# Optimization experiments

Measured on AMD Instinct MI355X. Metric: run time of the kernel, lower is better.

## Reference

```python
import jax, jax.numpy as jnp
import numpy as np


def _conv1x1(x, W, b):
    # 1x1 conv == per-pixel linear: x [B,H,W,Cin] @ W [Cin,Cout] + b
    return jnp.einsum('bhwc,cd->bhwd', x, W) + b


def setup_inputs() -> dict:
    key = jax.random.key(0)
    ks = jax.random.split(key, 5)
    B, H, W, C = 4, 64, 64, 256
    Ck = C // 8
    x = jax.random.normal(ks[0], (B, H, W, C), dtype=jnp.float32)
    Wf = jax.random.normal(ks[1], (C, Ck), dtype=jnp.float32) * 0.05
    Wg = jax.random.normal(ks[2], (C, Ck), dtype=jnp.float32) * 0.05
    Wh = jax.random.normal(ks[3], (C, C), dtype=jnp.float32) * 0.05
    Wv = jax.random.normal(ks[4], (C, C), dtype=jnp.float32) * 0.05
    return {
        'x': x,
        'Wf': Wf, 'bf': jnp.zeros((Ck,), jnp.float32),
        'Wg': Wg, 'bg': jnp.zeros((Ck,), jnp.float32),
        'Wh': Wh, 'bh': jnp.zeros((C,), jnp.float32),
        'Wv': Wv, 'bv': jnp.zeros((C,), jnp.float32),
    }


def reference(x, Wf, bf, Wg, bg, Wh, bh, Wv, bv):
    B, H, W, C = x.shape
    f = _conv1x1(x, Wf, bf).reshape(B, H * W, -1)   # [B,N,C/8]
    g = _conv1x1(x, Wg, bg).reshape(B, H * W, -1)   # [B,N,C/8]
    hm = _conv1x1(x, Wh, bh).reshape(B, H * W, C)   # [B,N,C]
    # unscaled attention: s = g @ f^T, softmax over last axis
    s = jnp.einsum('bnk,bmk->bnm', g, f)            # [B,N,N]
    beta = jax.nn.softmax(s, axis=-1)
    o = jnp.einsum('bnm,bmc->bnc', beta, hm)        # [B,N,C]
    o = o.reshape(B, H, W, C)
    o = _conv1x1(o, Wv, bv)
    return x + o
```

## Files before the change

### kernel.cpp

```cpp
#include <hip/hip_runtime.h>
#include <math.h>


typedef unsigned short u16;
typedef __attribute__((ext_vector_type(8))) short  bf16x8;
typedef __attribute__((ext_vector_type(4))) float  f32x4;

__device__ inline u16 f2bf(float x) {
    unsigned u = __float_as_uint(x);
    unsigned r = (u + 0x7fffu + ((u >> 16) & 1u)) >> 16;
    return (u16)r;
}

__device__ inline float bf2f(short s) {
    return __uint_as_float(((unsigned)(u16)s) << 16);
}

__device__ inline bf16x8 cvt8(float4 a, float4 b) {
    bf16x8 r;
    r[0] = (short)f2bf(a.x); r[1] = (short)f2bf(a.y);
    r[2] = (short)f2bf(a.z); r[3] = (short)f2bf(a.w);
    r[4] = (short)f2bf(b.x); r[5] = (short)f2bf(b.y);
    r[6] = (short)f2bf(b.z); r[7] = (short)f2bf(b.w);
    return r;
}

#define ASYNC_CP16(gp, lp)                                                     \
    __builtin_amdgcn_global_load_lds(                                          \
        (const __attribute__((address_space(1))) void*)(gp),                   \
        (__attribute__((address_space(3))) void*)(lp), 16, 0, 0)

#define LOG2E 1.4426950408889634f

__device__ inline size_t vfrag_off(int b, int cg, int kc, int quad, int l16) {
    return ((((size_t)b * 16 + cg) * 128 + kc) << 9) + (quad << 7) + (l16 << 3);
}

__global__ __launch_bounds__(256) void prep_w2(
    const float* __restrict__ Wf, const float* __restrict__ Wg,
    const float* __restrict__ Wh, const float* __restrict__ Wv,
    u16* __restrict__ wT)
{
    __shared__ float ldsw[256 * 33];

    const int bid = blockIdx.x;
    const int t   = threadIdx.x;

    const float* src;
    int cs, c0, nbase;
    float scale = 1.f;
    if (bid == 0)       { src = Wf; cs = 32;  c0 = 0;               nbase = 0; }
    else if (bid == 1)  { src = Wg; cs = 32;  c0 = 0;               nbase = 32;  scale = LOG2E; }
    else if (bid < 10)  { src = Wh; cs = 256; c0 = (bid - 2) * 32;  nbase = 64  + (bid - 2) * 32; }
    else                { src = Wv; cs = 256; c0 = (bid - 10) * 32; nbase = 320 + (bid - 10) * 32; }

#pragma unroll
    for (int i = 0; i < 32; ++i) {
        int idx = i * 256 + t;
        int k = idx >> 5;
        int n = idx & 31;
        ldsw[k * 33 + n] = src[(size_t)k * cs + c0 + n];
    }
    __syncthreads();

#pragma unroll
    for (int i = 0; i < 32; ++i) {
        int idx = i * 256 + t;
        int n = idx >> 8;
        int k = idx & 255;
        wT[(size_t)(nbase + n) * 256 + k] = f2bf(ldsw[k * 33 + n] * scale);
    }
}

__global__ __launch_bounds__(256) void proj_mfma2(
    const float* __restrict__ x, const u16* __restrict__ wT,
    const float* __restrict__ bfv, const float* __restrict__ bgv,
    const float* __restrict__ bhv,
    u16* __restrict__ fg, u16* __restrict__ hmt)
{
    __shared__ float xl[16 * 268];

    const int t    = threadIdx.x;
    const int w    = t >> 6;
    const int lane = t & 63;
    const int quad = lane >> 4;
    const int l16  = lane & 15;
    const int m0   = blockIdx.x * 16;
    const int wb   = w * 80;

#pragma unroll
    for (int i = 0; i < 4; ++i) {
        int idx = i * 256 + t;
        int row = idx >> 6;
        int c4  = (idx & 63) << 2;
        float4 v = *reinterpret_cast<const float4*>(
            x + (size_t)(m0 + row) * 256 + c4);
        *reinterpret_cast<float4*>(&xl[row * 268 + c4]) = v;
    }
    __syncthreads();

    f32x4 acc[5];
#pragma unroll
    for (int nt = 0; nt < 5; ++nt)
#pragma unroll
        for (int r = 0; r < 4; ++r) acc[nt][r] = 0.f;

#pragma unroll 2
    for (int ks = 0; ks < 8; ++ks) {
        const float* xp = &xl[l16 * 268 + ks * 32 + quad * 8];
        float4 a0 = *reinterpret_cast<const float4*>(xp);
        float4 a1 = *reinterpret_cast<const float4*>(xp + 4);
        bf16x8 afrag = cvt8(a0, a1);
#pragma unroll
        for (int nt = 0; nt < 5; ++nt) {
            bf16x8 bfrag = *reinterpret_cast<const bf16x8*>(
                wT + (size_t)(wb + nt * 16 + l16) * 256 + ks * 32 + quad * 8);
            acc[nt] = __builtin_amdgcn_mfma_f32_16x16x32_bf16(
                afrag, bfrag, acc[nt], 0, 0, 0);
        }
    }

    const int bb   = m0 >> 12;
    const int npix = m0 & 4095;
#pragma unroll
    for (int nt = 0; nt < 5; ++nt) {
        int col = wb + nt * 16 + l16;
        if (col < 64) {
            float bias = (col < 32) ? bfv[col] : bgv[col - 32] * LOG2E;
            int row = m0 + quad * 4;
#pragma unroll
            for (int r = 0; r < 4; ++r)
                fg[(size_t)(row + r) * 64 + col] = f2bf(acc[nt][r] + bias);
        } else {
            int c = col - 64;
            float bias = bhv[c];
            int n0 = npix + quad * 4;
            ushort4 hv;
            hv.x = f2bf(acc[nt][0] + bias);
            hv.y = f2bf(acc[nt][1] + bias);
            hv.z = f2bf(acc[nt][2] + bias);
            hv.w = f2bf(acc[nt][3] + bias);
            size_t off = ((((size_t)bb * 16 + (c >> 4)) * 128 + (n0 >> 5))
                          << 9) + (((n0 >> 3) & 3) << 7) + ((c & 15) << 3) +
                         (n0 & 7);
            *reinterpret_cast<ushort4*>(hmt + off) = hv;
        }
    }
}

__global__ __launch_bounds__(256) void attn5(
    const u16* __restrict__ fg, const u16* __restrict__ hmt,
    u16* __restrict__ obf, float* __restrict__ lpart, int ksl)
{
    __shared__ u16 fl[2][4096];
    __shared__ u16 pl[8192];

    const int t    = threadIdx.x;
    const int w    = t >> 6;
    const int lane = t & 63;
    const int quad = lane >> 4;
    const int l16  = lane & 15;

    int b, qt, ks;
    if (ksl == 1) {
        const int u   = blockIdx.x;
        const int xcd = u & 7;
        b = xcd >> 1;
        const int v = ((u >> 3) << 1) | (xcd & 1);
        qt = v >> 1;
        ks = v & 1;
    } else {
        ks = 0;
        qt = blockIdx.x & 63;
        b  = blockIdx.x >> 6;
    }
    const int nkt = 32 >> ksl;
    const int kt0 = ks * nkt;

    const size_t fg_base = (size_t)b * 4096 * 64;

    const bf16x8 gfrag = *reinterpret_cast<const bf16x8*>(
        fg + fg_base + (size_t)(qt * 64 + w * 16 + l16) * 64 + 32 + quad * 8);

    f32x4 oacc[4][4];
#pragma unroll
    for (int mt = 0; mt < 4; ++mt)
#pragma unroll
        for (int nt = 0; nt < 4; ++nt)
#pragma unroll
            for (int r = 0; r < 4; ++r) oacc[mt][nt][r] = 0.f;

    float lsum[4] = {0.f, 0.f, 0.f, 0.f};
    const f32x4 zero4 = {0.f, 0.f, 0.f, 0.f};

    {
        const u16* gp = fg + fg_base +
            (size_t)(kt0 * 128 + (2 * w) * 16 + l16) * 64 + quad * 8;
        ASYNC_CP16(gp, &fl[0][(2 * w) * 512]);
        ASYNC_CP16(gp + 16 * 64, &fl[0][(2 * w + 1) * 512]);
    }

    for (int it = 0; it < nkt; ++it) {
        const int kt  = kt0 + it;
        const int buf = it & 1;
        __syncthreads();

        bf16x8 vbr[4][4];
#pragma unroll
        for (int nt = 0; nt < 4; ++nt)
#pragma unroll
            for (int kh = 0; kh < 4; ++kh)
                vbr[nt][kh] = *reinterpret_cast<const bf16x8*>(
                    hmt + vfrag_off(b, w * 4 + nt, kt * 4 + kh, quad, l16));

        if (it + 1 < nkt) {
            const u16* gp = fg + fg_base +
                (size_t)((kt + 1) * 128 + (2 * w) * 16 + l16) * 64 + quad * 8;
            ASYNC_CP16(gp, &fl[buf ^ 1][(2 * w) * 512]);
            ASYNC_CP16(gp + 16 * 64, &fl[buf ^ 1][(2 * w + 1) * 512]);
        }

        f32x4 sacc[8];
#pragma unroll
        for (int ct = 0; ct < 8; ++ct) {
            bf16x8 fb = *reinterpret_cast<const bf16x8*>(
                &fl[buf][ct * 512 + quad * 128 + l16 * 8]);
            sacc[ct] = __builtin_amdgcn_mfma_f32_16x16x32_bf16(
                gfrag, fb, zero4, 0, 0, 0);
        }

#pragma unroll
        for (int ct = 0; ct < 8; ++ct) {
#pragma unroll
            for (int r = 0; r < 4; ++r) {
                float p = __builtin_amdgcn_exp2f(sacc[ct][r]);
                lsum[r] += p;
                int row = w * 16 + quad * 4 + r;
                int key = ct * 16 + l16;
                pl[(key >> 3) * 512 + row * 8 + (key & 7)] = f2bf(p);
            }
        }
        __syncthreads();

#pragma unroll
        for (int kh = 0; kh < 4; ++kh) {
            bf16x8 pa[4];
#pragma unroll
            for (int mt = 0; mt < 4; ++mt)
                pa[mt] = *reinterpret_cast<const bf16x8*>(
                    &pl[(kh * 4 + quad) * 512 + (mt * 16 + l16) * 8]);
#pragma unroll
            for (int nt = 0; nt < 4; ++nt)
#pragma unroll
                for (int mt = 0; mt < 4; ++mt)
                    oacc[mt][nt] = __builtin_amdgcn_mfma_f32_16x16x32_bf16(
                        pa[mt], vbr[nt][kh], oacc[mt][nt], 0, 0, 0);
        }
    }

#pragma unroll
    for (int r = 0; r < 4; ++r) {
        float s = lsum[r];
        s += __shfl_xor(s, 1);
        s += __shfl_xor(s, 2);
        s += __shfl_xor(s, 4);
        s += __shfl_xor(s, 8);
        lsum[r] = s;
    }
    if (l16 == 0) {
#pragma unroll
        for (int r = 0; r < 4; ++r)
            lpart[((size_t)ks << 14) + b * 4096 + qt * 64 + w * 16 +
                  quad * 4 + r] = lsum[r];
    }

#pragma unroll
    for (int mt = 0; mt < 4; ++mt) {
        const int row16 = b * 256 + qt * 4 + mt;
#pragma unroll
        for (int nt = 0; nt < 4; ++nt) {
            int ksc = w * 2 + (nt >> 1);
            int qc  = (nt & 1) * 2 + (l16 >> 3);
            u16* op = obf + ((size_t)ks << 22) +
                (((size_t)row16 * 8 + ksc) << 9) + (qc << 7) + (l16 & 7);
#pragma unroll
            for (int r = 0; r < 4; ++r)
                op[(quad * 4 + r) * 8] = f2bf(oacc[mt][nt][r]);
        }
    }
}

__global__ __launch_bounds__(256, 2) void attn8(
    const u16* __restrict__ fg, const u16* __restrict__ hmt,
    u16* __restrict__ obf, float* __restrict__ lpart, int ksl)
{
    __shared__ u16 fl[2][4096];
    __shared__ u16 pl[16 * 1024];

    const int t    = threadIdx.x;
    const int w    = t >> 6;
    const int lane = t & 63;
    const int quad = lane >> 4;
    const int l16  = lane & 15;

    const int u   = blockIdx.x;
    const int xcd = u & 7;
    const int b   = xcd >> 1;
    const int v   = ((u >> 3) << 1) | (xcd & 1);
    const int qt  = v >> ksl;
    const int ks  = v & ((1 << ksl) - 1);

    const int nkt = 32 >> ksl;
    const int kt0 = ks * nkt;

    const size_t fg_base = (size_t)b * 4096 * 64;

    bf16x8 gfrag[2];
#pragma unroll
    for (int h2 = 0; h2 < 2; ++h2)
        gfrag[h2] = *reinterpret_cast<const bf16x8*>(
            fg + fg_base +
            (size_t)(qt * 128 + w * 32 + h2 * 16 + l16) * 64 + 32 + quad * 8);

    f32x4 oacc[8][4];
#pragma unroll
    for (int mt = 0; mt < 8; ++mt)
#pragma unroll
        for (int nt = 0; nt < 4; ++nt)
#pragma unroll
            for (int r = 0; r < 4; ++r) oacc[mt][nt][r] = 0.f;

    float lsum[2][4] = {{0.f, 0.f, 0.f, 0.f}, {0.f, 0.f, 0.f, 0.f}};
    const f32x4 zero4 = {0.f, 0.f, 0.f, 0.f};

    {
        const u16* gp = fg + fg_base +
            (size_t)(kt0 * 128 + (2 * w) * 16 + l16) * 64 + quad * 8;
        ASYNC_CP16(gp, &fl[0][(2 * w) * 512]);
        ASYNC_CP16(gp + 16 * 64, &fl[0][(2 * w + 1) * 512]);
    }

    for (int it = 0; it < nkt; ++it) {
        const int kt  = kt0 + it;
        const int buf = it & 1;
        __syncthreads();

        if (it + 1 < nkt) {
            const u16* gp = fg + fg_base +
                (size_t)((kt + 1) * 128 + (2 * w) * 16 + l16) * 64 + quad * 8;
            ASYNC_CP16(gp, &fl[buf ^ 1][(2 * w) * 512]);
            ASYNC_CP16(gp + 16 * 64, &fl[buf ^ 1][(2 * w + 1) * 512]);
        }

        {
            f32x4 sacc[8];
#pragma unroll
            for (int ct = 0; ct < 8; ++ct) {
                bf16x8 fb = *reinterpret_cast<const bf16x8*>(
                    &fl[buf][ct * 512 + quad * 128 + l16 * 8]);
                sacc[ct] = __builtin_amdgcn_mfma_f32_16x16x32_bf16(
                    gfrag[0], fb, zero4, 0, 0, 0);
            }
#pragma unroll
            for (int ct = 0; ct < 8; ++ct) {
#pragma unroll
                for (int r = 0; r < 4; ++r) {
                    float p = __builtin_amdgcn_exp2f(sacc[ct][r]);
                    lsum[0][r] += p;
                    int row = w * 32 + quad * 4 + r;
                    int key = ct * 16 + l16;
                    pl[(key >> 3) * 1024 + row * 8 + (key & 7)] = f2bf(p);
                }
            }
        }

        bf16x8 va[4][2];
#pragma unroll
        for (int nt = 0; nt < 4; ++nt)
#pragma unroll
            for (int j = 0; j < 2; ++j)
                va[nt][j] = *reinterpret_cast<const bf16x8*>(
                    hmt + vfrag_off(b, w * 4 + nt, kt * 4 + j, quad, l16));

        {
            f32x4 sacc[8];
#pragma unroll
            for (int ct = 0; ct < 8; ++ct) {
                bf16x8 fb = *reinterpret_cast<const bf16x8*>(
                    &fl[buf][ct * 512 + quad * 128 + l16 * 8]);
                sacc[ct] = __builtin_amdgcn_mfma_f32_16x16x32_bf16(
                    gfrag[1], fb, zero4, 0, 0, 0);
            }
#pragma unroll
            for (int ct = 0; ct < 8; ++ct) {
#pragma unroll
                for (int r = 0; r < 4; ++r) {
                    float p = __builtin_amdgcn_exp2f(sacc[ct][r]);
                    lsum[1][r] += p;
                    int row = w * 32 + 16 + quad * 4 + r;
                    int key = ct * 16 + l16;
                    pl[(key >> 3) * 1024 + row * 8 + (key & 7)] = f2bf(p);
                }
            }
        }
        __syncthreads();

#pragma unroll
        for (int kh = 0; kh < 2; ++kh) {
#pragma unroll
            for (int mh = 0; mh < 2; ++mh) {
                bf16x8 pa[4];
#pragma unroll
                for (int m = 0; m < 4; ++m)
                    pa[m] = *reinterpret_cast<const bf16x8*>(
                        &pl[(kh * 4 + quad) * 1024 +
                            ((mh * 4 + m) * 16 + l16) * 8]);
#pragma unroll
                for (int nt = 0; nt < 4; ++nt)
#pragma unroll
                    for (int m = 0; m < 4; ++m)
                        oacc[mh * 4 + m][nt] =
                            __builtin_amdgcn_mfma_f32_16x16x32_bf16(
                                pa[m], va[nt][kh], oacc[mh * 4 + m][nt],
                                0, 0, 0);
            }
        }

        bf16x8 vb[4][2];
#pragma unroll
        for (int nt = 0; nt < 4; ++nt)
#pragma unroll
            for (int j = 0; j < 2; ++j)
                vb[nt][j] = *reinterpret_cast<const bf16x8*>(
                    hmt + vfrag_off(b, w * 4 + nt, kt * 4 + 2 + j, quad, l16));
#pragma unroll
        for (int kh = 2; kh < 4; ++kh) {
#pragma unroll
            for (int mh = 0; mh < 2; ++mh) {
                bf16x8 pa[4];
#pragma unroll
                for (int m = 0; m < 4; ++m)
                    pa[m] = *reinterpret_cast<const bf16x8*>(
                        &pl[(kh * 4 + quad) * 1024 +
                            ((mh * 4 + m) * 16 + l16) * 8]);
#pragma unroll
                for (int nt = 0; nt < 4; ++nt)
#pragma unroll
                    for (int m = 0; m < 4; ++m)
                        oacc[mh * 4 + m][nt] =
                            __builtin_amdgcn_mfma_f32_16x16x32_bf16(
                                pa[m], vb[nt][kh - 2], oacc[mh * 4 + m][nt],
                                0, 0, 0);
            }
        }
    }

#pragma unroll
    for (int h2 = 0; h2 < 2; ++h2) {
#pragma unroll
        for (int r = 0; r < 4; ++r) {
            float s = lsum[h2][r];
            s += __shfl_xor(s, 1);
            s += __shfl_xor(s, 2);
            s += __shfl_xor(s, 4);
            s += __shfl_xor(s, 8);
            lsum[h2][r] = s;
        }
    }
    if (l16 == 0) {
#pragma unroll
        for (int h2 = 0; h2 < 2; ++h2)
#pragma unroll
            for (int r = 0; r < 4; ++r) {
                int row = w * 32 + h2 * 16 + quad * 4 + r;
                lpart[((size_t)ks << 14) + b * 4096 + qt * 128 + row] =
                    lsum[h2][r];
            }
    }

#pragma unroll
    for (int mt = 0; mt < 8; ++mt) {
        const int row16 = b * 256 + qt * 8 + mt;
#pragma unroll
        for (int nt = 0; nt < 4; ++nt) {
            int ksc = w * 2 + (nt >> 1);
            int qc  = (nt & 1) * 2 + (l16 >> 3);
            u16* op = obf + ((size_t)ks << 22) +
                (((size_t)row16 * 8 + ksc) << 9) + (qc << 7) + (l16 & 7);
#pragma unroll
            for (int r = 0; r < 4; ++r)
                op[(quad * 4 + r) * 8] = f2bf(oacc[mt][nt][r]);
        }
    }
}

__global__ __launch_bounds__(256) void final_mfma8(
    const u16* __restrict__ obf, const float* __restrict__ lpart, int S,
    const u16* __restrict__ wT, const float* __restrict__ bvv,
    const float* __restrict__ x, float* __restrict__ out)
{
    __shared__ u16 ol[16384];
    __shared__ float linv[16];

    const int t    = threadIdx.x;
    const int w    = t >> 6;
    const int lane = t & 63;
    const int quad = lane >> 4;
    const int l16  = lane & 15;
    const int m0   = blockIdx.x * 16;
    const int wb   = w * 64;

    const int ni = S * 2;
    for (int i = 0; i < ni; ++i) {
        int gi = w * ni + i;
        int s  = gi >> 3;
        int ks = gi & 7;
        const u16* gp = obf + ((size_t)s << 22) +
            (((size_t)(m0 >> 4) * 8 + ks) << 9) + lane * 8;
        ASYNC_CP16(gp, &ol[gi * 512]);
    }

    if (t < 16) {
        float tot = 0.f;
#pragma unroll
        for (int s = 0; s < 4; ++s)
            if (s < S) tot += lpart[((size_t)s << 14) + m0 + t];
        linv[t] = 1.f / tot;
    }
    __syncthreads();

    f32x4 acc[4];
#pragma unroll
    for (int nt = 0; nt < 4; ++nt)
#pragma unroll
        for (int r = 0; r < 4; ++r) acc[nt][r] = 0.f;

#pragma unroll 2
    for (int ks = 0; ks < 8; ++ks) {
        bf16x8 afrag;
        {
            bf16x8 v0 = *reinterpret_cast<const bf16x8*>(
                &ol[ks * 512 + lane * 8]);
            if (S == 1) {
                afrag = v0;
            } else {
                float tacc[8];
#pragma unroll
                for (int j = 0; j < 8; ++j) tacc[j] = bf2f(v0[j]);
#pragma unroll
                for (int s = 1; s < 4; ++s) {
                    if (s < S) {
                        bf16x8 vs = *reinterpret_cast<const bf16x8*>(
                            &ol[(s * 8 + ks) * 512 + lane * 8]);
#pragma unroll
                        for (int j = 0; j < 8; ++j)
                            tacc[j] += bf2f(vs[j]);
                    }
                }
#pragma unroll
                for (int j = 0; j < 8; ++j) afrag[j] = (short)f2bf(tacc[j]);
            }
        }
#pragma unroll
        for (int nt = 0; nt < 4; ++nt) {
            bf16x8 bfrag = *reinterpret_cast<const bf16x8*>(
                wT + (size_t)(320 + wb + nt * 16 + l16) * 256 +
                ks * 32 + quad * 8);
            acc[nt] = __builtin_amdgcn_mfma_f32_16x16x32_bf16(
                afrag, bfrag, acc[nt], 0, 0, 0);
        }
    }

#pragma unroll
    for (int nt = 0; nt < 4; ++nt) {
        int col = wb + nt * 16 + l16;
        float bias = bvv[col];
        int row = m0 + quad * 4;
#pragma unroll
        for (int r = 0; r < 4; ++r) {
            size_t off = (size_t)(row + r) * 256 + col;
            out[off] = acc[nt][r] * linv[quad * 4 + r] + bias + x[off];
        }
    }
}

extern "C" void kernel_launch(void* const* d_in, const int* in_sizes, int n_in,
                              void* d_out, int out_size, void* d_ws, size_t ws_size,
                              hipStream_t stream)
{
    const float* x  = (const float*)d_in[0];
    const float* Wf = (const float*)d_in[1];
    const float* bf = (const float*)d_in[2];
    const float* Wg = (const float*)d_in[3];
    const float* bg = (const float*)d_in[4];
    const float* Wh = (const float*)d_in[5];
    const float* bh = (const float*)d_in[6];
    const float* Wv = (const float*)d_in[7];
    const float* bv = (const float*)d_in[8];
    float* out = (float*)d_out;

    const int M = 16384;

    const size_t base_b = (size_t)M * 64 * 2 + (size_t)4 * 256 * 4096 * 2 +
                          (size_t)576 * 256 * 2;
    const size_t per_s  = (size_t)M * 4 + (size_t)M * 256 * 2;
    int ksl = 0;
    if (ws_size >= base_b + 4 * per_s)      ksl = 2;
    else if (ws_size >= base_b + 2 * per_s) ksl = 1;
    const int S = 1 << ksl;

    u16*   fgbuf = (u16*)d_ws;
    u16*   hmt   = fgbuf + (size_t)M * 64;
    u16*   wT    = hmt + (size_t)4 * 256 * 4096;
    float* lpart = (float*)(wT + (size_t)576 * 256);
    u16*   obf   = (u16*)(lpart + (size_t)S * M);

    dim3 blk(256);

    prep_w2<<<dim3(18), blk, 0, stream>>>(Wf, Wg, Wh, Wv, wT);
    proj_mfma2<<<dim3(M / 16), blk, 0, stream>>>(x, wT, bf, bg, bh, fgbuf, hmt);
    if (ksl == 2)
        attn8<<<dim3(512), blk, 0, stream>>>(fgbuf, hmt, obf, lpart, ksl);
    else
        attn5<<<dim3(256 * S), blk, 0, stream>>>(fgbuf, hmt, obf, lpart, ksl);
    final_mfma8<<<dim3(M / 16), blk, 0, stream>>>(
        obf, lpart, S, wT, bv, x, out);
}
```

Measured before the change: 172.9 us.

## Fuse all four stages into one cooperative persistent kernel with grid syncs

Replaces the four separate launches (weight prep, projection, attention, output projection) with a single cooperative kernel of 512 blocks that separates stages with grid-wide syncs. Each block handles two 16-row tiles in the projection and final stages, so a grid of the same size as the attention stage covers everything. This is meant to remove per-launch overhead and the drain gaps between kernels. In exchange it adds grid-sync cost, needs all 512 blocks co-resident (2 per CU on 256 CUs), and carries the attention stage's register and LDS footprint through every stage. It falls back to the old launches if cooperative launch is unavailable or fails.

```diff
diff --git a/kernel.cpp b/kernel.cpp
--- a/kernel.cpp
+++ b/kernel.cpp
@@ -1,5 +1,8 @@
 #include <hip/hip_runtime.h>
+#include <hip/hip_cooperative_groups.h>
 #include <math.h>
+
+namespace cg = cooperative_groups;
 
 
 typedef unsigned short u16;
@@ -36,38 +39,420 @@
     return ((((size_t)b * 16 + cg) * 128 + kc) << 9) + (quad << 7) + (l16 << 3);
 }
 
+__global__ __launch_bounds__(256, 2) void fused4(
+    const float* __restrict__ x,
+    const float* __restrict__ Wf, const float* __restrict__ bfv,
+    const float* __restrict__ Wg, const float* __restrict__ bgv,
+    const float* __restrict__ Wh, const float* __restrict__ bhv,
+    const float* __restrict__ Wv, const float* __restrict__ bvv,
+    u16* __restrict__ fg, u16* __restrict__ hmt, u16* __restrict__ wT,
+    float* __restrict__ lpart, u16* __restrict__ obf,
+    float* __restrict__ out)
+{
+    __shared__ __align__(16) unsigned char smem[49152];
+    cg::grid_group grid = cg::this_grid();
+
+    const int bid  = blockIdx.x;
+    const int t    = threadIdx.x;
+    const int w    = t >> 6;
+    const int lane = t & 63;
+    const int quad = lane >> 4;
+    const int l16  = lane & 15;
+
+    if (bid < 18) {
+        float* ldsw = (float*)smem;
+        const float* src; int cs, c0, nbase; float scale = 1.f;
+        if (bid == 0)      { src = Wf; cs = 32;  c0 = 0;             nbase = 0; }
+        else if (bid == 1) { src = Wg; cs = 32;  c0 = 0;             nbase = 32; scale = LOG2E; }
+        else if (bid < 10) { src = Wh; cs = 256; c0 = (bid-2)*32;    nbase = 64  + (bid-2)*32; }
+        else               { src = Wv; cs = 256; c0 = (bid-10)*32;   nbase = 320 + (bid-10)*32; }
+#pragma unroll
+        for (int i = 0; i < 32; ++i) {
+            int idx = i * 256 + t;
+            int k = idx >> 5, n = idx & 31;
+            ldsw[k * 33 + n] = src[(size_t)k * cs + c0 + n];
+        }
+        __syncthreads();
+#pragma unroll
+        for (int i = 0; i < 32; ++i) {
+            int idx = i * 256 + t;
+            int n = idx >> 8, k = idx & 255;
+            wT[(size_t)(nbase + n) * 256 + k] = f2bf(ldsw[k * 33 + n] * scale);
+        }
+    }
+    grid.sync();
+
+    {
+        float* xl = (float*)smem;
+        const int wb = w * 80;
+        for (int h2 = 0; h2 < 2; ++h2) {
+            const int m0 = bid * 32 + h2 * 16;
+            __syncthreads();
+#pragma unroll
+            for (int i = 0; i < 4; ++i) {
+                int idx = i * 256 + t;
+                int row = idx >> 6;
+                int c4  = (idx & 63) << 2;
+                float4 v = *reinterpret_cast<const float4*>(
+                    x + (size_t)(m0 + row) * 256 + c4);
+                *reinterpret_cast<float4*>(&xl[row * 268 + c4]) = v;
+            }
+            __syncthreads();
+
+            f32x4 acc[5];
+#pragma unroll
+            for (int nt = 0; nt < 5; ++nt)
+#pragma unroll
+                for (int r = 0; r < 4; ++r) acc[nt][r] = 0.f;
+
+#pragma unroll 2
+            for (int ks = 0; ks < 8; ++ks) {
+                const float* xp = &xl[l16 * 268 + ks * 32 + quad * 8];
+                float4 a0 = *reinterpret_cast<const float4*>(xp);
+                float4 a1 = *reinterpret_cast<const float4*>(xp + 4);
+                bf16x8 afrag = cvt8(a0, a1);
+#pragma unroll
+                for (int nt = 0; nt < 5; ++nt) {
+                    bf16x8 bfrag = *reinterpret_cast<const bf16x8*>(
+                        wT + (size_t)(wb + nt * 16 + l16) * 256 +
+                        ks * 32 + quad * 8);
+                    acc[nt] = __builtin_amdgcn_mfma_f32_16x16x32_bf16(
+                        afrag, bfrag, acc[nt], 0, 0, 0);
+                }
+            }
+
+            const int bb   = m0 >> 12;
+            const int npix = m0 & 4095;
+#pragma unroll
+            for (int nt = 0; nt < 5; ++nt) {
+                int col = wb + nt * 16 + l16;
+                if (col < 64) {
+                    float bias = (col < 32) ? bfv[col] : bgv[col - 32] * LOG2E;
+                    int row = m0 + quad * 4;
+#pragma unroll
+                    for (int r = 0; r < 4; ++r)
+                        fg[(size_t)(row + r) * 64 + col] =
+                            f2bf(acc[nt][r] + bias);
+                } else {
+                    int c = col - 64;
+                    float bias = bhv[c];
+                    int n0 = npix + quad * 4;
+                    ushort4 hv;
+                    hv.x = f2bf(acc[nt][0] + bias);
+                    hv.y = f2bf(acc[nt][1] + bias);
+                    hv.z = f2bf(acc[nt][2] + bias);
+                    hv.w = f2bf(acc[nt][3] + bias);
+                    size_t off = ((((size_t)bb * 16 + (c >> 4)) * 128 +
+                                   (n0 >> 5)) << 9) +
+                                 (((n0 >> 3) & 3) << 7) + ((c & 15) << 3) +
+                                 (n0 & 7);
+                    *reinterpret_cast<ushort4*>(hmt + off) = hv;
+                }
+            }
+        }
+    }
+    grid.sync();
+
+    {
+        u16* fl = (u16*)smem;
+        u16* pl = (u16*)smem + 8192;
+
+        const int xcd = bid & 7;
+        const int b   = xcd >> 1;
+        const int v   = ((bid >> 3) << 1) | (xcd & 1);
+        const int qt  = v >> 2;
+        const int ks  = v & 3;
+        const int nkt = 8;
+        const int kt0 = ks * 8;
+
+        const size_t fg_base = (size_t)b * 4096 * 64;
+
+        bf16x8 gfrag[2];
+#pragma unroll
+        for (int h2 = 0; h2 < 2; ++h2)
+            gfrag[h2] = *reinterpret_cast<const bf16x8*>(
+                fg + fg_base +
+                (size_t)(qt * 128 + w * 32 + h2 * 16 + l16) * 64 + 32 +
+                quad * 8);
+
+        f32x4 oacc[8][4];
+#pragma unroll
+        for (int mt = 0; mt < 8; ++mt)
+#pragma unroll
+            for (int nt = 0; nt < 4; ++nt)
+#pragma unroll
+                for (int r = 0; r < 4; ++r) oacc[mt][nt][r] = 0.f;
+
+        float lsum[2][4] = {{0.f, 0.f, 0.f, 0.f}, {0.f, 0.f, 0.f, 0.f}};
+        const f32x4 zero4 = {0.f, 0.f, 0.f, 0.f};
+
+        {
+            const u16* gp = fg + fg_base +
+                (size_t)(kt0 * 128 + (2 * w) * 16 + l16) * 64 + quad * 8;
+            ASYNC_CP16(gp, fl + (2 * w) * 512);
+            ASYNC_CP16(gp + 16 * 64, fl + (2 * w + 1) * 512);
+        }
+
+        for (int it = 0; it < nkt; ++it) {
+            const int kt  = kt0 + it;
+            const int buf = it & 1;
+            __syncthreads();
+
+            if (it + 1 < nkt) {
+                const u16* gp = fg + fg_base +
+                    (size_t)((kt + 1) * 128 + (2 * w) * 16 + l16) * 64 +
+                    quad * 8;
+                ASYNC_CP16(gp, fl + (buf ^ 1) * 4096 + (2 * w) * 512);
+                ASYNC_CP16(gp + 16 * 64,
+                           fl + (buf ^ 1) * 4096 + (2 * w + 1) * 512);
+            }
+
+            {
+                f32x4 sacc[8];
+#pragma unroll
+                for (int ct = 0; ct < 8; ++ct) {
+                    bf16x8 fb = *reinterpret_cast<const bf16x8*>(
+                        &fl[buf * 4096 + ct * 512 + quad * 128 + l16 * 8]);
+                    sacc[ct] = __builtin_amdgcn_mfma_f32_16x16x32_bf16(
+                        gfrag[0], fb, zero4, 0, 0, 0);
+                }
+#pragma unroll
+                for (int ct = 0; ct < 8; ++ct) {
+#pragma unroll
+                    for (int r = 0; r < 4; ++r) {
+                        float p = __builtin_amdgcn_exp2f(sacc[ct][r]);
+                        lsum[0][r] += p;
+                        int row = w * 32 + quad * 4 + r;
+                        int key = ct * 16 + l16;
+                        pl[(key >> 3) * 1024 + row * 8 + (key & 7)] = f2bf(p);
+                    }
+                }
+            }
+
+            bf16x8 va[4][2];
+#pragma unroll
+            for (int nt = 0; nt < 4; ++nt)
+#pragma unroll
+                for (int j = 0; j < 2; ++j)
+                    va[nt][j] = *reinterpret_cast<const bf16x8*>(
+                        hmt + vfrag_off(b, w * 4 + nt, kt * 4 + j, quad, l16));
+
+            {
+                f32x4 sacc[8];
+#pragma unroll
+                for (int ct = 0; ct < 8; ++ct) {
+                    bf16x8 fb = *reinterpret_cast<const bf16x8*>(
+                        &fl[buf * 4096 + ct * 512 + quad * 128 + l16 * 8]);
+                    sacc[ct] = __builtin_amdgcn_mfma_f32_16x16x32_bf16(
+                        gfrag[1], fb, zero4, 0, 0, 0);
+                }
+#pragma unroll
+                for (int ct = 0; ct < 8; ++ct) {
+#pragma unroll
+                    for (int r = 0; r < 4; ++r) {
+                        float p = __builtin_amdgcn_exp2f(sacc[ct][r]);
+                        lsum[1][r] += p;
+                        int row = w * 32 + 16 + quad * 4 + r;
+                        int key = ct * 16 + l16;
+                        pl[(key >> 3) * 1024 + row * 8 + (key & 7)] = f2bf(p);
+                    }
+                }
+            }
+            __syncthreads();
+
+#pragma unroll
+            for (int kh = 0; kh < 2; ++kh) {
+#pragma unroll
+                for (int mh = 0; mh < 2; ++mh) {
+                    bf16x8 pa[4];
+#pragma unroll
+                    for (int m = 0; m < 4; ++m)
+                        pa[m] = *reinterpret_cast<const bf16x8*>(
+                            &pl[(kh * 4 + quad) * 1024 +
+                                ((mh * 4 + m) * 16 + l16) * 8]);
+#pragma unroll
+                    for (int nt = 0; nt < 4; ++nt)
+#pragma unroll
+                        for (int m = 0; m < 4; ++m)
+                            oacc[mh * 4 + m][nt] =
+                                __builtin_amdgcn_mfma_f32_16x16x32_bf16(
+                                    pa[m], va[nt][kh], oacc[mh * 4 + m][nt],
+                                    0, 0, 0);
+                }
+            }
+
+            bf16x8 vb[4][2];
+#pragma unroll
+            for (int nt = 0; nt < 4; ++nt)
+#pragma unroll
+                for (int j = 0; j < 2; ++j)
+                    vb[nt][j] = *reinterpret_cast<const bf16x8*>(
+                        hmt + vfrag_off(b, w * 4 + nt, kt * 4 + 2 + j,
+                                        quad, l16));
+#pragma unroll
+            for (int kh = 2; kh < 4; ++kh) {
+#pragma unroll
+                for (int mh = 0; mh < 2; ++mh) {
+                    bf16x8 pa[4];
+#pragma unroll
+                    for (int m = 0; m < 4; ++m)
+                        pa[m] = *reinterpret_cast<const bf16x8*>(
+                            &pl[(kh * 4 + quad) * 1024 +
+                                ((mh * 4 + m) * 16 + l16) * 8]);
+#pragma unroll
+                    for (int nt = 0; nt < 4; ++nt)
+#pragma unroll
+                        for (int m = 0; m < 4; ++m)
+                            oacc[mh * 4 + m][nt] =
+                                __builtin_amdgcn_mfma_f32_16x16x32_bf16(
+                                    pa[m], vb[nt][kh - 2],
+                                    oacc[mh * 4 + m][nt], 0, 0, 0);
+                }
+            }
+        }
+
+#pragma unroll
+        for (int h2 = 0; h2 < 2; ++h2) {
+#pragma unroll
+            for (int r = 0; r < 4; ++r) {
+                float s = lsum[h2][r];
+                s += __shfl_xor(s, 1);
+                s += __shfl_xor(s, 2);
+                s += __shfl_xor(s, 4);
+                s += __shfl_xor(s, 8);
+                lsum[h2][r] = s;
+            }
+        }
+        if (l16 == 0) {
+#pragma unroll
+            for (int h2 = 0; h2 < 2; ++h2)
+#pragma unroll
+                for (int r = 0; r < 4; ++r) {
+                    int row = w * 32 + h2 * 16 + quad * 4 + r;
+                    lpart[((size_t)ks << 14) + b * 4096 + qt * 128 + row] =
+                        lsum[h2][r];
+                }
+        }
+
+#pragma unroll
+        for (int mt = 0; mt < 8; ++mt) {
+            const int row16 = b * 256 + qt * 8 + mt;
+#pragma unroll
+            for (int nt = 0; nt < 4; ++nt) {
+                int ksc = w * 2 + (nt >> 1);
+                int qc  = (nt & 1) * 2 + (l16 >> 3);
+                u16* op = obf + ((size_t)ks << 22) +
+                    (((size_t)row16 * 8 + ksc) << 9) + (qc << 7) + (l16 & 7);
+#pragma unroll
+                for (int r = 0; r < 4; ++r)
+                    op[(quad * 4 + r) * 8] = f2bf(oacc[mt][nt][r]);
+            }
+        }
+    }
+    grid.sync();
+
+    {
+        u16*   ol   = (u16*)smem;
+        float* linv = (float*)(smem + 32768);
+        const int wb = w * 64;
+
+        for (int h2 = 0; h2 < 2; ++h2) {
+            const int m0 = bid * 32 + h2 * 16;
+            __syncthreads();
+
+            for (int i = 0; i < 8; ++i) {
+                int gi = w * 8 + i;
+                int s  = gi >> 3;
+                int ks = gi & 7;
+                const u16* gp = obf + ((size_t)s << 22) +
+                    (((size_t)(m0 >> 4) * 8 + ks) << 9) + lane * 8;
+                ASYNC_CP16(gp, ol + gi * 512);
+            }
+
+            if (t < 16) {
+                float tot = 0.f;
+#pragma unroll
+                for (int s = 0; s < 4; ++s)
+                    tot += lpart[((size_t)s << 14) + m0 + t];
+                linv[t] = 1.f / tot;
+            }
+            __syncthreads();
+
+            f32x4 acc[4];
+#pragma unroll
+            for (int nt = 0; nt < 4; ++nt)
+#pragma unroll
+                for (int r = 0; r < 4; ++r) acc[nt][r] = 0.f;
+
+#pragma unroll 2
+            for (int ks = 0; ks < 8; ++ks) {
+                bf16x8 afrag;
+                {
+                    bf16x8 v0 = *reinterpret_cast<const bf16x8*>(
+                        &ol[ks * 512 + lane * 8]);
+                    float tacc[8];
+#pragma unroll
+                    for (int j = 0; j < 8; ++j) tacc[j] = bf2f(v0[j]);
+#pragma unroll
+                    for (int s = 1; s < 4; ++s) {
+                        bf16x8 vs = *reinterpret_cast<const bf16x8*>(
+                            &ol[(s * 8 + ks) * 512 + lane * 8]);
+#pragma unroll
+                        for (int j = 0; j < 8; ++j) tacc[j] += bf2f(vs[j]);
+                    }
+#pragma unroll
+                    for (int j = 0; j < 8; ++j)
+                        afrag[j] = (short)f2bf(tacc[j]);
+                }
+#pragma unroll
+                for (int nt = 0; nt < 4; ++nt) {
+                    bf16x8 bfrag = *reinterpret_cast<const bf16x8*>(
+                        wT + (size_t)(320 + wb + nt * 16 + l16) * 256 +
+                        ks * 32 + quad * 8);
+                    acc[nt] = __builtin_amdgcn_mfma_f32_16x16x32_bf16(
+                        afrag, bfrag, acc[nt], 0, 0, 0);
+                }
+            }
+
+#pragma unroll
+            for (int nt = 0; nt < 4; ++nt) {
+                int col = wb + nt * 16 + l16;
+                float bias = bvv[col];
+                int row = m0 + quad * 4;
+#pragma unroll
+                for (int r = 0; r < 4; ++r) {
+                    size_t off = (size_t)(row + r) * 256 + col;
+                    out[off] = acc[nt][r] * linv[quad * 4 + r] + bias + x[off];
+                }
+            }
+        }
+    }
+}
+
 __global__ __launch_bounds__(256) void prep_w2(
     const float* __restrict__ Wf, const float* __restrict__ Wg,
     const float* __restrict__ Wh, const float* __restrict__ Wv,
     u16* __restrict__ wT)
 {
     __shared__ float ldsw[256 * 33];
-
     const int bid = blockIdx.x;
     const int t   = threadIdx.x;
-
-    const float* src;
-    int cs, c0, nbase;
-    float scale = 1.f;
-    if (bid == 0)       { src = Wf; cs = 32;  c0 = 0;               nbase = 0; }
-    else if (bid == 1)  { src = Wg; cs = 32;  c0 = 0;               nbase = 32;  scale = LOG2E; }
-    else if (bid < 10)  { src = Wh; cs = 256; c0 = (bid - 2) * 32;  nbase = 64  + (bid - 2) * 32; }
-    else                { src = Wv; cs = 256; c0 = (bid - 10) * 32; nbase = 320 + (bid - 10) * 32; }
-
+    const float* src; int cs, c0, nbase; float scale = 1.f;
+    if (bid == 0)      { src = Wf; cs = 32;  c0 = 0;             nbase = 0; }
+    else if (bid == 1) { src = Wg; cs = 32;  c0 = 0;             nbase = 32; scale = LOG2E; }
+    else if (bid < 10) { src = Wh; cs = 256; c0 = (bid-2)*32;    nbase = 64  + (bid-2)*32; }
+    else               { src = Wv; cs = 256; c0 = (bid-10)*32;   nbase = 320 + (bid-10)*32; }
 #pragma unroll
     for (int i = 0; i < 32; ++i) {
         int idx = i * 256 + t;
-        int k = idx >> 5;
-        int n = idx & 31;
+        int k = idx >> 5, n = idx & 31;
         ldsw[k * 33 + n] = src[(size_t)k * cs + c0 + n];
     }
     __syncthreads();
-
 #pragma unroll
     for (int i = 0; i < 32; ++i) {
         int idx = i * 256 + t;
-        int n = idx >> 8;
-        int k = idx & 255;
+        int n = idx >> 8, k = idx & 255;
         wT[(size_t)(nbase + n) * 256 + k] = f2bf(ldsw[k * 33 + n] * scale);
     }
 }
@@ -79,7 +464,6 @@
     u16* __restrict__ fg, u16* __restrict__ hmt)
 {
     __shared__ float xl[16 * 268];
-
     const int t    = threadIdx.x;
     const int w    = t >> 6;
     const int lane = t & 63;
@@ -87,7 +471,6 @@
     const int l16  = lane & 15;
     const int m0   = blockIdx.x * 16;
     const int wb   = w * 80;
-
 #pragma unroll
     for (int i = 0; i < 4; ++i) {
         int idx = i * 256 + t;
@@ -98,13 +481,11 @@
         *reinterpret_cast<float4*>(&xl[row * 268 + c4]) = v;
     }
     __syncthreads();
-
     f32x4 acc[5];
 #pragma unroll
     for (int nt = 0; nt < 5; ++nt)
 #pragma unroll
         for (int r = 0; r < 4; ++r) acc[nt][r] = 0.f;
-
 #pragma unroll 2
     for (int ks = 0; ks < 8; ++ks) {
         const float* xp = &xl[l16 * 268 + ks * 32 + quad * 8];
@@ -119,7 +500,6 @@
                 afrag, bfrag, acc[nt], 0, 0, 0);
         }
     }
-
     const int bb   = m0 >> 12;
     const int npix = m0 & 4095;
 #pragma unroll
@@ -154,13 +534,11 @@
 {
     __shared__ u16 fl[2][4096];
     __shared__ u16 pl[8192];
-
     const int t    = threadIdx.x;
     const int w    = t >> 6;
     const int lane = t & 63;
     const int quad = lane >> 4;
     const int l16  = lane & 15;
-
     int b, qt, ks;
     if (ksl == 1) {
         const int u   = blockIdx.x;
@@ -176,12 +554,9 @@
     }
     const int nkt = 32 >> ksl;
     const int kt0 = ks * nkt;
-
     const size_t fg_base = (size_t)b * 4096 * 64;
-
     const bf16x8 gfrag = *reinterpret_cast<const bf16x8*>(
         fg + fg_base + (size_t)(qt * 64 + w * 16 + l16) * 64 + 32 + quad * 8);
-
     f32x4 oacc[4][4];
 #pragma unroll
     for (int mt = 0; mt < 4; ++mt)
@@ -189,22 +564,18 @@
         for (int nt = 0; nt < 4; ++nt)
 #pragma unroll
             for (int r = 0; r < 4; ++r) oacc[mt][nt][r] = 0.f;
-
     float lsum[4] = {0.f, 0.f, 0.f, 0.f};
     const f32x4 zero4 = {0.f, 0.f, 0.f, 0.f};
-
     {
         const u16* gp = fg + fg_base +
             (size_t)(kt0 * 128 + (2 * w) * 16 + l16) * 64 + quad * 8;
         ASYNC_CP16(gp, &fl[0][(2 * w) * 512]);
         ASYNC_CP16(gp + 16 * 64, &fl[0][(2 * w + 1) * 512]);
     }
-
     for (int it = 0; it < nkt; ++it) {
         const int kt  = kt0 + it;
         const int buf = it & 1;
         __syncthreads();
-
         bf16x8 vbr[4][4];
 #pragma unroll
         for (int nt = 0; nt < 4; ++nt)
@@ -212,14 +583,12 @@
             for (int kh = 0; kh < 4; ++kh)
                 vbr[nt][kh] = *reinterpret_cast<const bf16x8*>(
                     hmt + vfrag_off(b, w * 4 + nt, kt * 4 + kh, quad, l16));
-
         if (it + 1 < nkt) {
             const u16* gp = fg + fg_base +
                 (size_t)((kt + 1) * 128 + (2 * w) * 16 + l16) * 64 + quad * 8;
             ASYNC_CP16(gp, &fl[buf ^ 1][(2 * w) * 512]);
             ASYNC_CP16(gp + 16 * 64, &fl[buf ^ 1][(2 * w + 1) * 512]);
         }
-
         f32x4 sacc[8];
 #pragma unroll
         for (int ct = 0; ct < 8; ++ct) {
@@ -228,7 +597,6 @@
             sacc[ct] = __builtin_amdgcn_mfma_f32_16x16x32_bf16(
                 gfrag, fb, zero4, 0, 0, 0);
         }
-
 #pragma unroll
         for (int ct = 0; ct < 8; ++ct) {
 #pragma unroll
@@ -241,7 +609,6 @@
             }
         }
         __syncthreads();
-
 #pragma unroll
         for (int kh = 0; kh < 4; ++kh) {
             bf16x8 pa[4];
@@ -257,7 +624,6 @@
                         pa[mt], vbr[nt][kh], oacc[mt][nt], 0, 0, 0);
         }
     }
-
 #pragma unroll
     for (int r = 0; r < 4; ++r) {
         float s = lsum[r];
@@ -273,7 +639,6 @@
             lpart[((size_t)ks << 14) + b * 4096 + qt * 64 + w * 16 +
                   quad * 4 + r] = lsum[r];
     }
-
 #pragma unroll
     for (int mt = 0; mt < 4; ++mt) {
         const int row16 = b * 256 + qt * 4 + mt;
@@ -296,32 +661,26 @@
 {
     __shared__ u16 fl[2][4096];
     __shared__ u16 pl[16 * 1024];
-
     const int t    = threadIdx.x;
     const int w    = t >> 6;
     const int lane = t & 63;
     const int quad = lane >> 4;
     const int l16  = lane & 15;
-
     const int u   = blockIdx.x;
     const int xcd = u & 7;
     const int b   = xcd >> 1;
     const int v   = ((u >> 3) << 1) | (xcd & 1);
     const int qt  = v >> ksl;
     const int ks  = v & ((1 << ksl) - 1);
-
     const int nkt = 32 >> ksl;
     const int kt0 = ks * nkt;
-
     const size_t fg_base = (size_t)b * 4096 * 64;
-
     bf16x8 gfrag[2];
 #pragma unroll
     for (int h2 = 0; h2 < 2; ++h2)
         gfrag[h2] = *reinterpret_cast<const bf16x8*>(
             fg + fg_base +
             (size_t)(qt * 128 + w * 32 + h2 * 16 + l16) * 64 + 32 + quad * 8);
-
     f32x4 oacc[8][4];
 #pragma unroll
     for (int mt = 0; mt < 8; ++mt)
@@ -329,29 +688,24 @@
         for (int nt = 0; nt < 4; ++nt)
 #pragma unroll
             for (int r = 0; r < 4; ++r) oacc[mt][nt][r] = 0.f;
-
     float lsum[2][4] = {{0.f, 0.f, 0.f, 0.f}, {0.f, 0.f, 0.f, 0.f}};
     const f32x4 zero4 = {0.f, 0.f, 0.f, 0.f};
-
     {
         const u16* gp = fg + fg_base +
             (size_t)(kt0 * 128 + (2 * w) * 16 + l16) * 64 + quad * 8;
         ASYNC_CP16(gp, &fl[0][(2 * w) * 512]);
         ASYNC_CP16(gp + 16 * 64, &fl[0][(2 * w + 1) * 512]);
     }
-
     for (int it = 0; it < nkt; ++it) {
         const int kt  = kt0 + it;
         const int buf = it & 1;
         __syncthreads();
-
         if (it + 1 < nkt) {
             const u16* gp = fg + fg_base +
                 (size_t)((kt + 1) * 128 + (2 * w) * 16 + l16) * 64 + quad * 8;
             ASYNC_CP16(gp, &fl[buf ^ 1][(2 * w) * 512]);
             ASYNC_CP16(gp + 16 * 64, &fl[buf ^ 1][(2 * w + 1) * 512]);
         }
-
         {
             f32x4 sacc[8];
 #pragma unroll
@@ -373,7 +727,6 @@
                 }
             }
         }
-
         bf16x8 va[4][2];
 #pragma unroll
         for (int nt = 0; nt < 4; ++nt)
@@ -381,7 +734,6 @@
             for (int j = 0; j < 2; ++j)
                 va[nt][j] = *reinterpret_cast<const bf16x8*>(
                     hmt + vfrag_off(b, w * 4 + nt, kt * 4 + j, quad, l16));
-
         {
             f32x4 sacc[8];
 #pragma unroll
@@ -404,7 +756,6 @@
             }
         }
         __syncthreads();
-
 #pragma unroll
         for (int kh = 0; kh < 2; ++kh) {
 #pragma unroll
@@ -425,7 +776,6 @@
                                 0, 0, 0);
             }
         }
-
         bf16x8 vb[4][2];
 #pragma unroll
         for (int nt = 0; nt < 4; ++nt)
@@ -454,7 +804,6 @@
             }
         }
     }
-
 #pragma unroll
     for (int h2 = 0; h2 < 2; ++h2) {
 #pragma unroll
@@ -477,7 +826,6 @@
                     lsum[h2][r];
             }
     }
-
 #pragma unroll
     for (int mt = 0; mt < 8; ++mt) {
         const int row16 = b * 256 + qt * 8 + mt;
@@ -501,7 +849,6 @@
 {
     __shared__ u16 ol[16384];
     __shared__ float linv[16];
-
     const int t    = threadIdx.x;
     const int w    = t >> 6;
     const int lane = t & 63;
@@ -509,7 +856,6 @@
     const int l16  = lane & 15;
     const int m0   = blockIdx.x * 16;
     const int wb   = w * 64;
-
     const int ni = S * 2;
     for (int i = 0; i < ni; ++i) {
         int gi = w * ni + i;
@@ -519,7 +865,6 @@
             (((size_t)(m0 >> 4) * 8 + ks) << 9) + lane * 8;
         ASYNC_CP16(gp, &ol[gi * 512]);
     }
-
     if (t < 16) {
         float tot = 0.f;
 #pragma unroll
@@ -528,13 +873,11 @@
         linv[t] = 1.f / tot;
     }
     __syncthreads();
-
     f32x4 acc[4];
 #pragma unroll
     for (int nt = 0; nt < 4; ++nt)
 #pragma unroll
         for (int r = 0; r < 4; ++r) acc[nt][r] = 0.f;
-
 #pragma unroll 2
     for (int ks = 0; ks < 8; ++ks) {
         bf16x8 afrag;
@@ -553,8 +896,7 @@
                         bf16x8 vs = *reinterpret_cast<const bf16x8*>(
                             &ol[(s * 8 + ks) * 512 + lane * 8]);
 #pragma unroll
-                        for (int j = 0; j < 8; ++j)
-                            tacc[j] += bf2f(vs[j]);
+                        for (int j = 0; j < 8; ++j) tacc[j] += bf2f(vs[j]);
                     }
                 }
 #pragma unroll
@@ -570,7 +912,6 @@
                 afrag, bfrag, acc[nt], 0, 0, 0);
         }
     }
-
 #pragma unroll
     for (int nt = 0; nt < 4; ++nt) {
         int col = wb + nt * 16 + l16;
@@ -617,6 +958,27 @@
 
     dim3 blk(256);
 
+    static int coop_ok = -1;
+    if (coop_ok < 0) {
+        int dev = 0;
+        hipGetDevice(&dev);
+        int v = 0;
+        hipDeviceGetAttribute(&v, hipDeviceAttributeCooperativeLaunch, dev);
+        coop_ok = v;
+    }
+
+    if (ksl == 2 && coop_ok) {
+        void* kargs[] = {
+            (void*)&x,  (void*)&Wf, (void*)&bf, (void*)&Wg, (void*)&bg,
+            (void*)&Wh, (void*)&bh, (void*)&Wv, (void*)&bv,
+            (void*)&fgbuf, (void*)&hmt, (void*)&wT, (void*)&lpart,
+            (void*)&obf, (void*)&out };
+        hipError_t err = hipLaunchCooperativeKernel(
+            reinterpret_cast<const void*>(&fused4), dim3(512), blk,
+            kargs, 0u, stream);
+        if (err == hipSuccess) return;
+    }
+
     prep_w2<<<dim3(18), blk, 0, stream>>>(Wf, Wg, Wh, Wv, wT);
     proj_mfma2<<<dim3(M / 16), blk, 0, stream>>>(x, wT, bf, bg, bh, fgbuf, hmt);
     if (ksl == 2)
```

After: 376.3 us. 2.18x slower.
